# Optimization experiments

Hardware: AMD Instinct MI355X
Metric: run time of the kernel (lower is better)

## Reference

```python
import jax, jax.numpy as jnp
import numpy as np

B, N, H = 32, 1024, 256
ALPHA = 0.2  # leaky relu slope
NEG_INF = -1e12


def setup_inputs() -> dict:
    key = jax.random.key(0)
    k1, k2, k3, k4, k5, k6 = jax.random.split(key, 6)
    inp = jax.random.normal(k1, (B, N, H), dtype=jnp.float32)
    A = (jax.random.uniform(k2, (B, N, N)) < 0.05).astype(jnp.float32)
    l = jnp.sort(jax.random.randint(k3, (B, 2), 0, N), axis=1)
    # xavier-uniform(gain=1.414) approximated; exact init values are irrelevant for correctness
    lim_w = 1.414 * np.sqrt(6.0 / (H + H))
    W_i = jax.random.uniform(k4, (H, H), minval=-lim_w, maxval=lim_w, dtype=jnp.float32)
    W_c = jax.random.uniform(k5, (H, H), minval=-lim_w, maxval=lim_w, dtype=jnp.float32)
    lim_a = 1.414 * np.sqrt(6.0 / (2 * H + 1))
    a = jax.random.uniform(k6, (2 * H, 1), minval=-lim_a, maxval=lim_a, dtype=jnp.float32)
    return {"inp": inp, "A": A, "l": l, "W_i": W_i, "W_c": W_c, "a": a}


def reference(inp, A, l, W_i, W_c, a):
    # eval mode: dropout is identity (training=False)
    n = inp.shape[1]
    h = inp.shape[2]
    Wh_i = jnp.einsum('bnh,he->bne', inp, W_i)
    Wh_c = jnp.einsum('bnh,he->bne', inp, W_c)
    # vectorized replacement of the per-batch Wh[index][i:j] = Wh_i[index][i:j] loop
    idx = jnp.arange(n)
    sel = (idx[None, :] >= l[:, 0:1]) & (idx[None, :] < l[:, 1:2])  # [B,N]
    Wh = jnp.where(sel[:, :, None], Wh_i, Wh_c)
    # additive attention scores
    Wh1 = Wh @ a[:h, :]  # [B,N,1]
    Wh2 = Wh @ a[h:, :]  # [B,N,1]
    A_ = A + jnp.eye(n, dtype=A.dtype)
    e = jax.nn.leaky_relu((Wh1 + jnp.swapaxes(Wh2, 1, 2)) * A_, ALPHA)
    att = jnp.where(A_ > 0, e, NEG_INF)
    att = jax.nn.softmax(att, axis=2)
    h_prime = jnp.einsum('bnm,bme->bne', att, Wh)
    return jax.nn.elu(h_prime)  # concat=True
```

## Files before the change

### kernel.cpp

```cpp
#include <hip/hip_runtime.h>
#include <hip/hip_bf16.h>
#include <stdint.h>

#define B_ 32
#define N_ 1024
#define H_ 256
#define PF_PITCH 520

typedef short bf16x8 __attribute__((ext_vector_type(8)));
typedef float floatx4 __attribute__((ext_vector_type(4)));

__device__ inline unsigned short f2bs(float x) {
    __hip_bfloat16 h = __float2bfloat16(x);
    return __builtin_bit_cast(unsigned short, h);
}

__global__ __launch_bounds__(256)
void k_uvec(const float* __restrict__ Wi, const float* __restrict__ Wc,
            const float* __restrict__ a, float* __restrict__ U) {
    int k = blockIdx.x;
    int t = threadIdx.x;
    float wi = Wi[k * H_ + t];
    float wc = Wc[k * H_ + t];
    float a1 = a[t], a2 = a[H_ + t];
    float p0 = wi * a1, p1 = wc * a1, p2 = wi * a2, p3 = wc * a2;
    for (int off = 32; off; off >>= 1) {
        p0 += __shfl_xor(p0, off);
        p1 += __shfl_xor(p1, off);
        p2 += __shfl_xor(p2, off);
        p3 += __shfl_xor(p3, off);
    }
    __shared__ float red[4][4];
    int w = t >> 6;
    if ((t & 63) == 0) { red[w][0] = p0; red[w][1] = p1; red[w][2] = p2; red[w][3] = p3; }
    __syncthreads();
    if (t == 0) {
        U[0 * H_ + k] = red[0][0] + red[1][0] + red[2][0] + red[3][0];
        U[1 * H_ + k] = red[0][1] + red[1][1] + red[2][1] + red[3][1];
        U[2 * H_ + k] = red[0][2] + red[1][2] + red[2][2] + red[3][2];
        U[3 * H_ + k] = red[0][3] + red[1][3] + red[2][3] + red[3][3];
    }
}

__global__ __launch_bounds__(256)
void k_prep(const float* __restrict__ Wi, const float* __restrict__ Wc,
            unsigned short* __restrict__ WtFi, unsigned short* __restrict__ WtFc) {
    __shared__ float tile[64][65];
    int mat = blockIdx.x >> 4;
    int tr = ((blockIdx.x >> 2) & 3) * 64;
    int tc = (blockIdx.x & 3) * 64;
    const float* W = mat ? Wc : Wi;
    unsigned short* WtF = mat ? WtFc : WtFi;
    int t = threadIdx.x;
    int rr = t >> 2, c4 = (t & 3) * 16;
    const float* src = W + (size_t)(tr + rr) * H_ + tc + c4;
#pragma unroll
    for (int j = 0; j < 4; ++j) {
        float4 v = *reinterpret_cast<const float4*>(src + j * 4);
        tile[rr][c4 + 4 * j + 0] = v.x;
        tile[rr][c4 + 4 * j + 1] = v.y;
        tile[rr][c4 + 4 * j + 2] = v.z;
        tile[rr][c4 + 4 * j + 3] = v.w;
    }
    __syncthreads();
#pragma unroll
    for (int h = 0; h < 2; ++h) {
        int s = h * 256 + t;
        int ksl = s >> 8;
        int cl  = (s >> 6) & 3;
        int ll  = s & 63;
        int m16v = ll & 15, quadv = ll >> 4;
        int nloc = cl * 16 + m16v;
        int kb = ksl * 32 + quadv * 8;
        unsigned int pk[4];
#pragma unroll
        for (int jj = 0; jj < 4; ++jj) {
            unsigned short lo = f2bs(tile[kb + 2 * jj][nloc]);
            unsigned short hi = f2bs(tile[kb + 2 * jj + 1][nloc]);
            pk[jj] = (unsigned int)lo | ((unsigned int)hi << 16);
        }
        int ksg = (tr >> 5) + ksl;
        int cg  = (tc >> 4) + cl;
        *reinterpret_cast<uint4*>(WtF + ((size_t)(ksg * 16 + cg) * 64 + ll) * 8) =
            *reinterpret_cast<uint4*>(pk);
    }
}

__global__ __launch_bounds__(256)
void k_gemm(const float* __restrict__ inp, const int* __restrict__ l,
            const unsigned short* __restrict__ WtFi, const unsigned short* __restrict__ WtFc,
            unsigned short* __restrict__ WhF, const float* __restrict__ U,
            float* __restrict__ Wh1, float* __restrict__ Wh2) {
    __shared__ unsigned short bbuf[2][4096];
    int blk = blockIdx.x;
    int b  = blk >> 5;
    int r0 = ((blk >> 1) & 15) * 64;
    int n0 = (blk & 1) * 128;
    int t = threadIdx.x;
    int w = t >> 6;
    int lane = t & 63;
    int quad = lane >> 4, m16 = lane & 15;
    int rowb = r0 + w * 16;

    int l0 = l[2 * b], l1 = l[2 * b + 1];
    bool allI = (l0 <= r0) && (r0 + 64 <= l1);
    bool allC = (l1 <= r0) || (l0 >= r0 + 64);
    int npass = (allI || allC) ? 1 : 2;

    int row = rowb + m16;
    bool sel = (row >= l0) && (row < l1);
    const float* xrow = inp + ((size_t)(b * N_ + row)) * H_;
    const float* u1 = U + (sel ? 0 : H_);
    const float* u2 = U + 2 * H_ + (sel ? 0 : H_);
    bool doWh = (n0 == 0);
    float d1 = 0.f, d2 = 0.f;

    unsigned short* fb = WhF + (size_t)b * (N_ * H_);
    int cb = n0 >> 4;

    int j0 = rowb + quad * 4;
    int ksO = j0 >> 5;
    int laneF = m16 + 16 * ((j0 & 31) >> 3);
    int jj0 = j0 & 7;

    for (int pass = 0; pass < npass; ++pass) {
        const unsigned short* WtF =
            (npass == 1) ? (allI ? WtFi : WtFc) : (pass == 0 ? WtFi : WtFc);
        const unsigned short* gbase = WtF + cb * 512;

        floatx4 acc[8];
#pragma unroll
        for (int c = 0; c < 8; ++c) acc[c] = (floatx4){0.f, 0.f, 0.f, 0.f};

        {
            uint4 v0 = *reinterpret_cast<const uint4*>(gbase + (size_t)t * 8);
            uint4 v1 = *reinterpret_cast<const uint4*>(gbase + (size_t)(256 + t) * 8);
            *reinterpret_cast<uint4*>(&bbuf[0][t * 8]) = v0;
            *reinterpret_cast<uint4*>(&bbuf[0][(256 + t) * 8]) = v1;
        }
        for (int ks = 0; ks < 8; ++ks) {
            __syncthreads();
            uint4 v0, v1;
            if (ks < 7) {
                v0 = *reinterpret_cast<const uint4*>(gbase + (size_t)(ks + 1) * 8192 + t * 8);
                v1 = *reinterpret_cast<const uint4*>(gbase + (size_t)(ks + 1) * 8192 + (256 + t) * 8);
            }
            const float4 xa = *reinterpret_cast<const float4*>(xrow + ks * 32 + quad * 8);
            const float4 xb = *reinterpret_cast<const float4*>(xrow + ks * 32 + quad * 8 + 4);
            if (pass == 0 && doWh) {
                const float4 ua = *reinterpret_cast<const float4*>(u1 + ks * 32 + quad * 8);
                const float4 ub = *reinterpret_cast<const float4*>(u1 + ks * 32 + quad * 8 + 4);
                const float4 va = *reinterpret_cast<const float4*>(u2 + ks * 32 + quad * 8);
                const float4 vb = *reinterpret_cast<const float4*>(u2 + ks * 32 + quad * 8 + 4);
                d1 += xa.x * ua.x + xa.y * ua.y + xa.z * ua.z + xa.w * ua.w
                    + xb.x * ub.x + xb.y * ub.y + xb.z * ub.z + xb.w * ub.w;
                d2 += xa.x * va.x + xa.y * va.y + xa.z * va.z + xa.w * va.w
                    + xb.x * vb.x + xb.y * vb.y + xb.z * vb.z + xb.w * vb.w;
            }
            unsigned int pk0 = (unsigned int)f2bs(xa.x) | ((unsigned int)f2bs(xa.y) << 16);
            unsigned int pk1 = (unsigned int)f2bs(xa.z) | ((unsigned int)f2bs(xa.w) << 16);
            unsigned int pk2 = (unsigned int)f2bs(xb.x) | ((unsigned int)f2bs(xb.y) << 16);
            unsigned int pk3 = (unsigned int)f2bs(xb.z) | ((unsigned int)f2bs(xb.w) << 16);
            uint4 apk = {pk0, pk1, pk2, pk3};
            bf16x8 af = __builtin_bit_cast(bf16x8, apk);

            const unsigned short* bptr = &bbuf[ks & 1][lane * 8];
#pragma unroll
            for (int c = 0; c < 8; ++c) {
                bf16x8 bfr = *reinterpret_cast<const bf16x8*>(bptr + c * 512);
                acc[c] = __builtin_amdgcn_mfma_f32_16x16x32_bf16(af, bfr, acc[c], 0, 0, 0);
            }
            if (ks < 7) {
                *reinterpret_cast<uint4*>(&bbuf[(ks + 1) & 1][t * 8]) = v0;
                *reinterpret_cast<uint4*>(&bbuf[(ks + 1) & 1][(256 + t) * 8]) = v1;
            }
        }
        __syncthreads();

#pragma unroll
        for (int c = 0; c < 8; ++c) {
            size_t base = ((size_t)((ksO * 16 + cb + c) * 64) + laneF) * 8 + jj0;
            if (npass == 1) {
                unsigned int lo = (unsigned int)f2bs(acc[c][0]) | ((unsigned int)f2bs(acc[c][1]) << 16);
                unsigned int hi = (unsigned int)f2bs(acc[c][2]) | ((unsigned int)f2bs(acc[c][3]) << 16);
                uint2 v = {lo, hi};
                *reinterpret_cast<uint2*>(fb + base) = v;
            } else {
                bool want[4]; bool all = true, none = true;
#pragma unroll
                for (int r = 0; r < 4; ++r) {
                    int j = j0 + r;
                    bool s2 = (j >= l0) && (j < l1);
                    want[r] = (pass == 0) ? s2 : !s2;
                    all = all && want[r]; none = none && !want[r];
                }
                if (all) {
                    unsigned int lo = (unsigned int)f2bs(acc[c][0]) | ((unsigned int)f2bs(acc[c][1]) << 16);
                    unsigned int hi = (unsigned int)f2bs(acc[c][2]) | ((unsigned int)f2bs(acc[c][3]) << 16);
                    uint2 v = {lo, hi};
                    *reinterpret_cast<uint2*>(fb + base) = v;
                } else if (!none) {
#pragma unroll
                    for (int r = 0; r < 4; ++r)
                        if (want[r]) fb[base + r] = f2bs(acc[c][r]);
                }
            }
        }
    }

    if (doWh) {
        d1 += __shfl_xor(d1, 16); d1 += __shfl_xor(d1, 32);
        d2 += __shfl_xor(d2, 16); d2 += __shfl_xor(d2, 32);
        if (quad == 0) {
            Wh1[b * N_ + rowb + m16] = d1;
            Wh2[b * N_ + rowb + m16] = d2;
        }
    }
}

__global__ __launch_bounds__(256)
void k_attn(const float* __restrict__ A, const float* __restrict__ Wh1,
            const float* __restrict__ Wh2, const unsigned short* __restrict__ WhF,
            float* __restrict__ out) {
    __shared__ unsigned short pfrag[2][32 * PF_PITCH];
    int t = threadIdx.x, w = t >> 6, lane = t & 63;
    int bi = blockIdx.x;
    int b = (bi & 7) * 4 + (bi >> 8);
    int tile = (bi >> 3) & 31;
    int rowbase = tile * 32;

    const float* Wh2b = Wh2 + b * N_;
    float4 w2v[4];
#pragma unroll
    for (int ch = 0; ch < 4; ++ch)
        w2v[ch] = *reinterpret_cast<const float4*>(Wh2b + ch * 256 + lane * 4);

    int ksl = lane >> 3;
    int q2 = (lane >> 1) & 3;
    int jj0 = (lane & 1) * 4;

#pragma unroll
    for (int tt = 0; tt < 2; ++tt) {
#pragma unroll
        for (int q = 0; q < 4; ++q) {
            int m = w * 4 + q;
            int i = rowbase + tt * 16 + m;
            float wh1 = Wh1[b * N_ + i];
            const float* Arow = A + ((size_t)(b * N_ + i)) * N_;
            int s = m + 16 * q2;
            int sw = s ^ ((s >> 3) & 7);
            int sls = sw * 8 + jj0;
#pragma unroll
            for (int ch = 0; ch < 4; ++ch) {
                float4 av = *reinterpret_cast<const float4*>(Arow + ch * 256 + lane * 4);
                if ((i >> 2) == (ch * 64 + lane)) ((float*)&av)[i & 3] += 1.0f;
                float aa[4] = {av.x, av.y, av.z, av.w};
                float ww[4] = {w2v[ch].x, w2v[ch].y, w2v[ch].z, w2v[ch].w};
                float p[4];
#pragma unroll
                for (int c = 0; c < 4; ++c) {
                    float e  = (wh1 + ww[c]) * aa[c];
                    float lv = fmaxf(e, 0.2f * e);
                    p[c] = aa[c] > 0.f ? __expf(lv) : 0.f;
                }
                unsigned int lo = (unsigned int)f2bs(p[0]) | ((unsigned int)f2bs(p[1]) << 16);
                unsigned int hi = (unsigned int)f2bs(p[2]) | ((unsigned int)f2bs(p[3]) << 16);
                uint2 v = {lo, hi};
                int ks = ch * 8 + ksl;
                *reinterpret_cast<uint2*>(pfrag[tt] + ks * PF_PITCH + sls) = v;
            }
        }
    }
    __syncthreads();

    const unsigned short* WB = WhF + (size_t)b * (N_ * H_);
    int rs = (lane ^ ((lane >> 3) & 7)) * 8;
    unsigned short oneb = f2bs(1.0f);
    bf16x8 bones = {(short)oneb, (short)oneb, (short)oneb, (short)oneb,
                    (short)oneb, (short)oneb, (short)oneb, (short)oneb};
    floatx4 acc0[4], acc1[4], sum0, sum1;
    sum0 = (floatx4){0.f, 0.f, 0.f, 0.f};
    sum1 = (floatx4){0.f, 0.f, 0.f, 0.f};
#pragma unroll
    for (int cc = 0; cc < 4; ++cc) {
        acc0[cc] = (floatx4){0.f, 0.f, 0.f, 0.f};
        acc1[cc] = (floatx4){0.f, 0.f, 0.f, 0.f};
    }
#pragma unroll 2
    for (int ks = 0; ks < 32; ++ks) {
        bf16x8 af0 = *reinterpret_cast<const bf16x8*>(pfrag[0] + ks * PF_PITCH + rs);
        bf16x8 af1 = *reinterpret_cast<const bf16x8*>(pfrag[1] + ks * PF_PITCH + rs);
        sum0 = __builtin_amdgcn_mfma_f32_16x16x32_bf16(af0, bones, sum0, 0, 0, 0);
        sum1 = __builtin_amdgcn_mfma_f32_16x16x32_bf16(af1, bones, sum1, 0, 0, 0);
#pragma unroll
        for (int cc = 0; cc < 4; ++cc) {
            int c = w * 4 + cc;
            bf16x8 bfv = *reinterpret_cast<const bf16x8*>(
                WB + ((size_t)((ks * 16 + c) * 64 + lane)) * 8);
            acc0[cc] = __builtin_amdgcn_mfma_f32_16x16x32_bf16(af0, bfv, acc0[cc], 0, 0, 0);
            acc1[cc] = __builtin_amdgcn_mfma_f32_16x16x32_bf16(af1, bfv, acc1[cc], 0, 0, 0);
        }
    }

    int quad = lane >> 4, m16 = lane & 15;
    float inv0[4], inv1[4];
#pragma unroll
    for (int r = 0; r < 4; ++r) {
        inv0[r] = 1.0f / sum0[r];
        inv1[r] = 1.0f / sum1[r];
    }
#pragma unroll
    for (int cc = 0; cc < 4; ++cc) {
        int col = (w * 4 + cc) * 16 + m16;
#pragma unroll
        for (int r = 0; r < 4; ++r) {
            int m = quad * 4 + r;
            float v0 = acc0[cc][r] * inv0[r];
            v0 = v0 > 0.f ? v0 : __expf(v0) - 1.0f;
            out[((size_t)(b * N_ + rowbase + m)) * H_ + col] = v0;
            float v1 = acc1[cc][r] * inv1[r];
            v1 = v1 > 0.f ? v1 : __expf(v1) - 1.0f;
            out[((size_t)(b * N_ + rowbase + 16 + m)) * H_ + col] = v1;
        }
    }
}

extern "C" void kernel_launch(void* const* d_in, const int* in_sizes, int n_in,
                              void* d_out, int out_size, void* d_ws, size_t ws_size,
                              hipStream_t stream) {
    const float* inp = (const float*)d_in[0];
    const float* A   = (const float*)d_in[1];
    const int*   l   = (const int*)d_in[2];
    const float* Wi  = (const float*)d_in[3];
    const float* Wc  = (const float*)d_in[4];
    const float* a   = (const float*)d_in[5];
    float* out = (float*)d_out;

    char* ws = (char*)d_ws;
    size_t off = 0;
    unsigned short* WhF  = (unsigned short*)(ws + off); off += (size_t)B_ * N_ * H_ * 2;
    float* Wh1 = (float*)(ws + off); off += (size_t)B_ * N_ * 4;
    float* Wh2 = (float*)(ws + off); off += (size_t)B_ * N_ * 4;
    float* U   = (float*)(ws + off); off += 4 * H_ * 4;
    unsigned short* WtFi = (unsigned short*)(ws + off); off += (size_t)H_ * H_ * 2;
    unsigned short* WtFc = (unsigned short*)(ws + off); off += (size_t)H_ * H_ * 2;

    k_uvec<<<H_, 256, 0, stream>>>(Wi, Wc, a, U);
    k_prep<<<32, 256, 0, stream>>>(Wi, Wc, WtFi, WtFc);
    k_gemm<<<B_ * 16 * 2, 256, 0, stream>>>(inp, l, WtFi, WtFc, WhF, U, Wh1, Wh2);
    k_attn<<<B_ * (N_ / 32), 256, 0, stream>>>(A, Wh1, Wh2, WhF, out);
}
```

Measured before the change: 280.9 us.

## Compute attention probabilities directly in MFMA register fragments, dropping LDS staging

The attention kernel no longer stages bf16 probability tiles in shared memory behind a block barrier. Each wave now handles 16 rows by 128 columns, builds its A-operand fragments in registers straight from the adjacency row and Wh2 inside the k-loop, and adds occupancy hints through launch bounds. This removes the LDS traffic and the barrier and lets softmax-numerator work overlap with the MFMAs. In exchange, two waves recompute the same probabilities (duplicate exp work), each WhF fragment is reused across only one row group instead of two, and A reads become per-lane strided rows rather than coalesced row sweeps.

```diff
diff --git a/kernel.cpp b/kernel.cpp
--- a/kernel.cpp
+++ b/kernel.cpp
@@ -5,7 +5,6 @@
 #define B_ 32
 #define N_ 1024
 #define H_ 256
-#define PF_PITCH 520
 
 typedef short bf16x8 __attribute__((ext_vector_type(8)));
 typedef float floatx4 __attribute__((ext_vector_type(4)));
@@ -218,109 +217,78 @@
     }
 }
 
-__global__ __launch_bounds__(256)
+__global__ __launch_bounds__(256, 4)
 void k_attn(const float* __restrict__ A, const float* __restrict__ Wh1,
             const float* __restrict__ Wh2, const unsigned short* __restrict__ WhF,
             float* __restrict__ out) {
-    __shared__ unsigned short pfrag[2][32 * PF_PITCH];
     int t = threadIdx.x, w = t >> 6, lane = t & 63;
+    int quad = lane >> 4, m16 = lane & 15;
     int bi = blockIdx.x;
     int b = (bi & 7) * 4 + (bi >> 8);
     int tile = (bi >> 3) & 31;
-    int rowbase = tile * 32;
-
-    const float* Wh2b = Wh2 + b * N_;
-    float4 w2v[4];
-#pragma unroll
-    for (int ch = 0; ch < 4; ++ch)
-        w2v[ch] = *reinterpret_cast<const float4*>(Wh2b + ch * 256 + lane * 4);
-
-    int ksl = lane >> 3;
-    int q2 = (lane >> 1) & 3;
-    int jj0 = (lane & 1) * 4;
-
-#pragma unroll
-    for (int tt = 0; tt < 2; ++tt) {
-#pragma unroll
-        for (int q = 0; q < 4; ++q) {
-            int m = w * 4 + q;
-            int i = rowbase + tt * 16 + m;
-            float wh1 = Wh1[b * N_ + i];
-            const float* Arow = A + ((size_t)(b * N_ + i)) * N_;
-            int s = m + 16 * q2;
-            int sw = s ^ ((s >> 3) & 7);
-            int sls = sw * 8 + jj0;
-#pragma unroll
-            for (int ch = 0; ch < 4; ++ch) {
-                float4 av = *reinterpret_cast<const float4*>(Arow + ch * 256 + lane * 4);
-                if ((i >> 2) == (ch * 64 + lane)) ((float*)&av)[i & 3] += 1.0f;
-                float aa[4] = {av.x, av.y, av.z, av.w};
-                float ww[4] = {w2v[ch].x, w2v[ch].y, w2v[ch].z, w2v[ch].w};
-                float p[4];
-#pragma unroll
-                for (int c = 0; c < 4; ++c) {
-                    float e  = (wh1 + ww[c]) * aa[c];
-                    float lv = fmaxf(e, 0.2f * e);
-                    p[c] = aa[c] > 0.f ? __expf(lv) : 0.f;
-                }
-                unsigned int lo = (unsigned int)f2bs(p[0]) | ((unsigned int)f2bs(p[1]) << 16);
-                unsigned int hi = (unsigned int)f2bs(p[2]) | ((unsigned int)f2bs(p[3]) << 16);
-                uint2 v = {lo, hi};
-                int ks = ch * 8 + ksl;
-                *reinterpret_cast<uint2*>(pfrag[tt] + ks * PF_PITCH + sls) = v;
-            }
-        }
-    }
-    __syncthreads();
-
-    const unsigned short* WB = WhF + (size_t)b * (N_ * H_);
-    int rs = (lane ^ ((lane >> 3) & 7)) * 8;
+    int rowtile = tile * 32 + (w & 1) * 16;
+    int ch = w >> 1;
+    int i = rowtile + m16;
+
+    float wh1 = Wh1[b * N_ + i];
+    const float* arow = A + ((size_t)(b * N_ + i)) * N_;
+    const float* w2b  = Wh2 + b * N_;
+    const unsigned short* WB = WhF + (size_t)b * (N_ * H_) + (size_t)(ch * 8) * 512;
+
     unsigned short oneb = f2bs(1.0f);
     bf16x8 bones = {(short)oneb, (short)oneb, (short)oneb, (short)oneb,
                     (short)oneb, (short)oneb, (short)oneb, (short)oneb};
-    floatx4 acc0[4], acc1[4], sum0, sum1;
-    sum0 = (floatx4){0.f, 0.f, 0.f, 0.f};
-    sum1 = (floatx4){0.f, 0.f, 0.f, 0.f};
-#pragma unroll
-    for (int cc = 0; cc < 4; ++cc) {
-        acc0[cc] = (floatx4){0.f, 0.f, 0.f, 0.f};
-        acc1[cc] = (floatx4){0.f, 0.f, 0.f, 0.f};
-    }
+    floatx4 acc[8], rsum = (floatx4){0.f, 0.f, 0.f, 0.f};
+#pragma unroll
+    for (int cc = 0; cc < 8; ++cc) acc[cc] = (floatx4){0.f, 0.f, 0.f, 0.f};
+
 #pragma unroll 2
     for (int ks = 0; ks < 32; ++ks) {
-        bf16x8 af0 = *reinterpret_cast<const bf16x8*>(pfrag[0] + ks * PF_PITCH + rs);
-        bf16x8 af1 = *reinterpret_cast<const bf16x8*>(pfrag[1] + ks * PF_PITCH + rs);
-        sum0 = __builtin_amdgcn_mfma_f32_16x16x32_bf16(af0, bones, sum0, 0, 0, 0);
-        sum1 = __builtin_amdgcn_mfma_f32_16x16x32_bf16(af1, bones, sum1, 0, 0, 0);
-#pragma unroll
-        for (int cc = 0; cc < 4; ++cc) {
-            int c = w * 4 + cc;
-            bf16x8 bfv = *reinterpret_cast<const bf16x8*>(
-                WB + ((size_t)((ks * 16 + c) * 64 + lane)) * 8);
-            acc0[cc] = __builtin_amdgcn_mfma_f32_16x16x32_bf16(af0, bfv, acc0[cc], 0, 0, 0);
-            acc1[cc] = __builtin_amdgcn_mfma_f32_16x16x32_bf16(af1, bfv, acc1[cc], 0, 0, 0);
-        }
-    }
-
-    int quad = lane >> 4, m16 = lane & 15;
-    float inv0[4], inv1[4];
-#pragma unroll
-    for (int r = 0; r < 4; ++r) {
-        inv0[r] = 1.0f / sum0[r];
-        inv1[r] = 1.0f / sum1[r];
-    }
-#pragma unroll
-    for (int cc = 0; cc < 4; ++cc) {
-        int col = (w * 4 + cc) * 16 + m16;
+        int j0 = ks * 32 + quad * 8;
+        float4 a0 = *reinterpret_cast<const float4*>(arow + j0);
+        float4 a1 = *reinterpret_cast<const float4*>(arow + j0 + 4);
+        float4 u0 = *reinterpret_cast<const float4*>(w2b + j0);
+        float4 u1 = *reinterpret_cast<const float4*>(w2b + j0 + 4);
+        float aa[8] = {a0.x, a0.y, a0.z, a0.w, a1.x, a1.y, a1.z, a1.w};
+        float uu[8] = {u0.x, u0.y, u0.z, u0.w, u1.x, u1.y, u1.z, u1.w};
+        unsigned int pk[4];
+#pragma unroll
+        for (int h2 = 0; h2 < 4; ++h2) {
+            float p2[2];
+#pragma unroll
+            for (int g = 0; g < 2; ++g) {
+                int jj = h2 * 2 + g;
+                float a_ = aa[jj] + ((j0 + jj) == i ? 1.0f : 0.0f);
+                float e  = (wh1 + uu[jj]) * a_;
+                float lv = fmaxf(e, 0.2f * e);
+                p2[g] = a_ > 0.f ? __expf(lv) : 0.f;
+            }
+            pk[h2] = (unsigned int)f2bs(p2[0]) | ((unsigned int)f2bs(p2[1]) << 16);
+        }
+        uint4 apk = {pk[0], pk[1], pk[2], pk[3]};
+        bf16x8 af = __builtin_bit_cast(bf16x8, apk);
+
+        rsum = __builtin_amdgcn_mfma_f32_16x16x32_bf16(af, bones, rsum, 0, 0, 0);
+        const unsigned short* bks = WB + (size_t)(ks * 16) * 512 + lane * 8;
+#pragma unroll
+        for (int cc = 0; cc < 8; ++cc) {
+            bf16x8 bfv = *reinterpret_cast<const bf16x8*>(bks + cc * 512);
+            acc[cc] = __builtin_amdgcn_mfma_f32_16x16x32_bf16(af, bfv, acc[cc], 0, 0, 0);
+        }
+    }
+
+    float inv[4];
+#pragma unroll
+    for (int r = 0; r < 4; ++r) inv[r] = 1.0f / rsum[r];
+#pragma unroll
+    for (int cc = 0; cc < 8; ++cc) {
+        int col = (ch * 8 + cc) * 16 + m16;
 #pragma unroll
         for (int r = 0; r < 4; ++r) {
             int m = quad * 4 + r;
-            float v0 = acc0[cc][r] * inv0[r];
-            v0 = v0 > 0.f ? v0 : __expf(v0) - 1.0f;
-            out[((size_t)(b * N_ + rowbase + m)) * H_ + col] = v0;
-            float v1 = acc1[cc][r] * inv1[r];
-            v1 = v1 > 0.f ? v1 : __expf(v1) - 1.0f;
-            out[((size_t)(b * N_ + rowbase + 16 + m)) * H_ + col] = v1;
+            float v = acc[cc][r] * inv[r];
+            v = v > 0.f ? v : __expf(v) - 1.0f;
+            out[((size_t)(b * N_ + rowtile + m)) * H_ + col] = v;
         }
     }
 }
```

Result: slower. 314.2 us (+11.9%).

## Halve attention row tile for occupancy and merge weight prep kernels

Applied to the files above, without the earlier changes.

The attention kernel now handles 16 rows per block instead of 32. This halves its LDS footprint and accumulator registers, doubles the grid, and adds launch_bounds(256,4) to allow more resident blocks. The two small preprocessing kernels are merged into one launch to save a kernel launch. In exchange, each WhF B-fragment is now read from global memory by twice as many blocks, so L2 traffic for Wh goes up.

```diff
diff --git a/kernel.cpp b/kernel.cpp
--- a/kernel.cpp
+++ b/kernel.cpp
@@ -16,42 +16,41 @@
 }
 
 __global__ __launch_bounds__(256)
-void k_uvec(const float* __restrict__ Wi, const float* __restrict__ Wc,
-            const float* __restrict__ a, float* __restrict__ U) {
-    int k = blockIdx.x;
+void k_pre(const float* __restrict__ Wi, const float* __restrict__ Wc,
+           const float* __restrict__ a,
+           unsigned short* __restrict__ WtFi, unsigned short* __restrict__ WtFc,
+           float* __restrict__ U) {
     int t = threadIdx.x;
-    float wi = Wi[k * H_ + t];
-    float wc = Wc[k * H_ + t];
-    float a1 = a[t], a2 = a[H_ + t];
-    float p0 = wi * a1, p1 = wc * a1, p2 = wi * a2, p3 = wc * a2;
-    for (int off = 32; off; off >>= 1) {
-        p0 += __shfl_xor(p0, off);
-        p1 += __shfl_xor(p1, off);
-        p2 += __shfl_xor(p2, off);
-        p3 += __shfl_xor(p3, off);
-    }
-    __shared__ float red[4][4];
-    int w = t >> 6;
-    if ((t & 63) == 0) { red[w][0] = p0; red[w][1] = p1; red[w][2] = p2; red[w][3] = p3; }
-    __syncthreads();
-    if (t == 0) {
-        U[0 * H_ + k] = red[0][0] + red[1][0] + red[2][0] + red[3][0];
-        U[1 * H_ + k] = red[0][1] + red[1][1] + red[2][1] + red[3][1];
-        U[2 * H_ + k] = red[0][2] + red[1][2] + red[2][2] + red[3][2];
-        U[3 * H_ + k] = red[0][3] + red[1][3] + red[2][3] + red[3][3];
-    }
-}
-
-__global__ __launch_bounds__(256)
-void k_prep(const float* __restrict__ Wi, const float* __restrict__ Wc,
-            unsigned short* __restrict__ WtFi, unsigned short* __restrict__ WtFc) {
+    if (blockIdx.x >= 32) {
+        int k = blockIdx.x - 32;
+        float wi = Wi[k * H_ + t];
+        float wc = Wc[k * H_ + t];
+        float a1 = a[t], a2 = a[H_ + t];
+        float p0 = wi * a1, p1 = wc * a1, p2 = wi * a2, p3 = wc * a2;
+        for (int off = 32; off; off >>= 1) {
+            p0 += __shfl_xor(p0, off);
+            p1 += __shfl_xor(p1, off);
+            p2 += __shfl_xor(p2, off);
+            p3 += __shfl_xor(p3, off);
+        }
+        __shared__ float red[4][4];
+        int w = t >> 6;
+        if ((t & 63) == 0) { red[w][0] = p0; red[w][1] = p1; red[w][2] = p2; red[w][3] = p3; }
+        __syncthreads();
+        if (t == 0) {
+            U[0 * H_ + k] = red[0][0] + red[1][0] + red[2][0] + red[3][0];
+            U[1 * H_ + k] = red[0][1] + red[1][1] + red[2][1] + red[3][1];
+            U[2 * H_ + k] = red[0][2] + red[1][2] + red[2][2] + red[3][2];
+            U[3 * H_ + k] = red[0][3] + red[1][3] + red[2][3] + red[3][3];
+        }
+        return;
+    }
     __shared__ float tile[64][65];
     int mat = blockIdx.x >> 4;
     int tr = ((blockIdx.x >> 2) & 3) * 64;
     int tc = (blockIdx.x & 3) * 64;
     const float* W = mat ? Wc : Wi;
     unsigned short* WtF = mat ? WtFc : WtFi;
-    int t = threadIdx.x;
     int rr = t >> 2, c4 = (t & 3) * 16;
     const float* src = W + (size_t)(tr + rr) * H_ + tc + c4;
 #pragma unroll
@@ -218,16 +217,17 @@
     }
 }
 
-__global__ __launch_bounds__(256)
+__global__ __launch_bounds__(256, 4)
 void k_attn(const float* __restrict__ A, const float* __restrict__ Wh1,
             const float* __restrict__ Wh2, const unsigned short* __restrict__ WhF,
             float* __restrict__ out) {
-    __shared__ unsigned short pfrag[2][32 * PF_PITCH];
+    __shared__ unsigned short pfrag[32 * PF_PITCH];
     int t = threadIdx.x, w = t >> 6, lane = t & 63;
+    int quad = lane >> 4, m16 = lane & 15;
     int bi = blockIdx.x;
-    int b = (bi & 7) * 4 + (bi >> 8);
-    int tile = (bi >> 3) & 31;
-    int rowbase = tile * 32;
+    int b = (bi & 7) * 4 + ((bi >> 3) >> 6);
+    int tile = (bi >> 3) & 63;
+    int rowbase = tile * 16;
 
     const float* Wh2b = Wh2 + b * N_;
     float4 w2v[4];
@@ -236,39 +236,36 @@
         w2v[ch] = *reinterpret_cast<const float4*>(Wh2b + ch * 256 + lane * 4);
 
     int ksl = lane >> 3;
-    int q2 = (lane >> 1) & 3;
+    int q2 = (lane & 7) >> 1;
     int jj0 = (lane & 1) * 4;
 
 #pragma unroll
-    for (int tt = 0; tt < 2; ++tt) {
-#pragma unroll
-        for (int q = 0; q < 4; ++q) {
-            int m = w * 4 + q;
-            int i = rowbase + tt * 16 + m;
-            float wh1 = Wh1[b * N_ + i];
-            const float* Arow = A + ((size_t)(b * N_ + i)) * N_;
-            int s = m + 16 * q2;
-            int sw = s ^ ((s >> 3) & 7);
-            int sls = sw * 8 + jj0;
-#pragma unroll
-            for (int ch = 0; ch < 4; ++ch) {
-                float4 av = *reinterpret_cast<const float4*>(Arow + ch * 256 + lane * 4);
-                if ((i >> 2) == (ch * 64 + lane)) ((float*)&av)[i & 3] += 1.0f;
-                float aa[4] = {av.x, av.y, av.z, av.w};
-                float ww[4] = {w2v[ch].x, w2v[ch].y, w2v[ch].z, w2v[ch].w};
-                float p[4];
-#pragma unroll
-                for (int c = 0; c < 4; ++c) {
-                    float e  = (wh1 + ww[c]) * aa[c];
-                    float lv = fmaxf(e, 0.2f * e);
-                    p[c] = aa[c] > 0.f ? __expf(lv) : 0.f;
-                }
-                unsigned int lo = (unsigned int)f2bs(p[0]) | ((unsigned int)f2bs(p[1]) << 16);
-                unsigned int hi = (unsigned int)f2bs(p[2]) | ((unsigned int)f2bs(p[3]) << 16);
-                uint2 v = {lo, hi};
-                int ks = ch * 8 + ksl;
-                *reinterpret_cast<uint2*>(pfrag[tt] + ks * PF_PITCH + sls) = v;
-            }
+    for (int q = 0; q < 4; ++q) {
+        int m = w * 4 + q;
+        int i = rowbase + m;
+        float wh1 = Wh1[b * N_ + i];
+        const float* Arow = A + ((size_t)(b * N_ + i)) * N_;
+        int s = m + 16 * q2;
+        int sw = s ^ ((s >> 3) & 7);
+        int sls = sw * 8 + jj0;
+#pragma unroll
+        for (int ch = 0; ch < 4; ++ch) {
+            float4 av = *reinterpret_cast<const float4*>(Arow + ch * 256 + lane * 4);
+            if ((i >> 2) == (ch * 64 + lane)) ((float*)&av)[i & 3] += 1.0f;
+            float aa[4] = {av.x, av.y, av.z, av.w};
+            float ww[4] = {w2v[ch].x, w2v[ch].y, w2v[ch].z, w2v[ch].w};
+            float p[4];
+#pragma unroll
+            for (int c = 0; c < 4; ++c) {
+                float e  = (wh1 + ww[c]) * aa[c];
+                float lv = fmaxf(e, 0.2f * e);
+                p[c] = aa[c] > 0.f ? __expf(lv) : 0.f;
+            }
+            unsigned int lo = (unsigned int)f2bs(p[0]) | ((unsigned int)f2bs(p[1]) << 16);
+            unsigned int hi = (unsigned int)f2bs(p[2]) | ((unsigned int)f2bs(p[3]) << 16);
+            uint2 v = {lo, hi};
+            int ks = ch * 8 + ksl;
+            *reinterpret_cast<uint2*>(pfrag + ks * PF_PITCH + sls) = v;
         }
     }
     __syncthreads();
@@ -278,49 +275,34 @@
     unsigned short oneb = f2bs(1.0f);
     bf16x8 bones = {(short)oneb, (short)oneb, (short)oneb, (short)oneb,
                     (short)oneb, (short)oneb, (short)oneb, (short)oneb};
-    floatx4 acc0[4], acc1[4], sum0, sum1;
-    sum0 = (floatx4){0.f, 0.f, 0.f, 0.f};
-    sum1 = (floatx4){0.f, 0.f, 0.f, 0.f};
-#pragma unroll
-    for (int cc = 0; cc < 4; ++cc) {
-        acc0[cc] = (floatx4){0.f, 0.f, 0.f, 0.f};
-        acc1[cc] = (floatx4){0.f, 0.f, 0.f, 0.f};
-    }
-#pragma unroll 2
+    floatx4 acc[4], rsum = (floatx4){0.f, 0.f, 0.f, 0.f};
+#pragma unroll
+    for (int cc = 0; cc < 4; ++cc) acc[cc] = (floatx4){0.f, 0.f, 0.f, 0.f};
+#pragma unroll 4
     for (int ks = 0; ks < 32; ++ks) {
-        bf16x8 af0 = *reinterpret_cast<const bf16x8*>(pfrag[0] + ks * PF_PITCH + rs);
-        bf16x8 af1 = *reinterpret_cast<const bf16x8*>(pfrag[1] + ks * PF_PITCH + rs);
-        sum0 = __builtin_amdgcn_mfma_f32_16x16x32_bf16(af0, bones, sum0, 0, 0, 0);
-        sum1 = __builtin_amdgcn_mfma_f32_16x16x32_bf16(af1, bones, sum1, 0, 0, 0);
+        bf16x8 af = *reinterpret_cast<const bf16x8*>(pfrag + ks * PF_PITCH + rs);
+        rsum = __builtin_amdgcn_mfma_f32_16x16x32_bf16(af, bones, rsum, 0, 0, 0);
 #pragma unroll
         for (int cc = 0; cc < 4; ++cc) {
             int c = w * 4 + cc;
             bf16x8 bfv = *reinterpret_cast<const bf16x8*>(
                 WB + ((size_t)((ks * 16 + c) * 64 + lane)) * 8);
-            acc0[cc] = __builtin_amdgcn_mfma_f32_16x16x32_bf16(af0, bfv, acc0[cc], 0, 0, 0);
-            acc1[cc] = __builtin_amdgcn_mfma_f32_16x16x32_bf16(af1, bfv, acc1[cc], 0, 0, 0);
-        }
-    }
-
-    int quad = lane >> 4, m16 = lane & 15;
-    float inv0[4], inv1[4];
-#pragma unroll
-    for (int r = 0; r < 4; ++r) {
-        inv0[r] = 1.0f / sum0[r];
-        inv1[r] = 1.0f / sum1[r];
-    }
+            acc[cc] = __builtin_amdgcn_mfma_f32_16x16x32_bf16(af, bfv, acc[cc], 0, 0, 0);
+        }
+    }
+
+    float inv[4];
+#pragma unroll
+    for (int r = 0; r < 4; ++r) inv[r] = 1.0f / rsum[r];
 #pragma unroll
     for (int cc = 0; cc < 4; ++cc) {
         int col = (w * 4 + cc) * 16 + m16;
 #pragma unroll
         for (int r = 0; r < 4; ++r) {
             int m = quad * 4 + r;
-            float v0 = acc0[cc][r] * inv0[r];
-            v0 = v0 > 0.f ? v0 : __expf(v0) - 1.0f;
-            out[((size_t)(b * N_ + rowbase + m)) * H_ + col] = v0;
-            float v1 = acc1[cc][r] * inv1[r];
-            v1 = v1 > 0.f ? v1 : __expf(v1) - 1.0f;
-            out[((size_t)(b * N_ + rowbase + 16 + m)) * H_ + col] = v1;
+            float v = acc[cc][r] * inv[r];
+            v = v > 0.f ? v : __expf(v) - 1.0f;
+            out[((size_t)(b * N_ + rowbase + m)) * H_ + col] = v;
         }
     }
 }
@@ -345,8 +327,7 @@
     unsigned short* WtFi = (unsigned short*)(ws + off); off += (size_t)H_ * H_ * 2;
     unsigned short* WtFc = (unsigned short*)(ws + off); off += (size_t)H_ * H_ * 2;
 
-    k_uvec<<<H_, 256, 0, stream>>>(Wi, Wc, a, U);
-    k_prep<<<32, 256, 0, stream>>>(Wi, Wc, WtFi, WtFc);
+    k_pre<<<288, 256, 0, stream>>>(Wi, Wc, a, WtFi, WtFc, U);
     k_gemm<<<B_ * 16 * 2, 256, 0, stream>>>(inp, l, WtFi, WtFc, WhF, U, Wh1, Wh2);
-    k_attn<<<B_ * (N_ / 32), 256, 0, stream>>>(A, Wh1, Wh2, WhF, out);
-}
+    k_attn<<<B_ * (N_ / 16), 256, 0, stream>>>(A, Wh1, Wh2, WhF, out);
+}
```

Result: slower. 287.3 us (+2.3%).
